# Kernel tuning notes

Hardware: AMD Instinct MI355X
Metric: run time of the kernel (lower is better)

## Reference

```python
import jax, jax.numpy as jnp
import numpy as np

B, T, N, C = 64, 8192, 16, 2
ONSET_PROB = 0.005  # sparse onsets, realistic for piano rolls


def setup_inputs() -> dict:
    key = jax.random.key(0)
    k1, k2 = jax.random.split(key)
    vals = jax.random.uniform(k1, (B, T, N, C), dtype=jnp.float32)
    mask = jax.random.uniform(k2, (B, T, N, 1)) < ONSET_PROB
    onsets = jnp.where(mask, vals, 0.0)  # mostly-zero onset roll
    return {"onsets": onsets}


def reference(onsets):
    # onsets: (b, t, n, c). onset flag per frame: any note's channel-0 > 0.
    b, t, n, c = onsets.shape
    onset = jnp.max(onsets[..., 0], axis=-1) > 0  # (b, t) bool
    # Recurrence state = (state + 1) * (1 - onset) counts frames since the
    # last onset (0 at an onset frame), with a virtual onset at index -1.
    # Closed form: out[i] = i - (index of most recent onset <= i, else -1).
    ar = jnp.arange(t, dtype=jnp.int32)  # (t,)
    idx = jnp.where(onset, ar[None, :], -1)  # (b, t)
    last = jax.lax.cummax(idx, axis=1)  # (b, t) last onset index so far
    out = (ar[None, :] - last).astype(onsets.dtype)[..., None]  # (b, t, 1)
    return out
```

## Files before the change

### kernel.cpp

```cpp
#include <hip/hip_runtime.h>

#define B_ 64
#define T_ 8192
#define N_ 16
#define C_ 2
#define TILE 256
#define NT (T_ / TILE)

__global__ __launch_bounds__(TILE) void k1_scan(const float* __restrict__ onsets,
                                                float* __restrict__ out,
                                                int* __restrict__ tileMax,
                                                int* __restrict__ firstOnset) {
    __shared__ int s[TILE];
    const int blk  = blockIdx.x;
    const int b    = blk / NT;
    const int tile = blk % NT;
    const int tid  = threadIdx.x;
    const int t    = tile * TILE + tid;

    const float4* p = (const float4*)onsets + (size_t)(b * T_ + t) * (N_ * C_ / 4);
    float m = 0.0f;
#pragma unroll
    for (int i = 0; i < 8; ++i) {
        float4 v = p[i];
        m = fmaxf(m, fmaxf(v.x, v.z));
    }
    const bool onset = (m > 0.0f);
    int idx = onset ? t : -1;

    s[tid] = idx;
    __syncthreads();
#pragma unroll
    for (int off = 1; off < TILE; off <<= 1) {
        int u = (tid >= off) ? s[tid - off] : -1;
        int v = s[tid];
        __syncthreads();
        s[tid] = (u > v) ? u : v;
        __syncthreads();
    }
    const int last = s[tid];
    out[b * T_ + t] = (float)(t - last);

    if (tid == TILE - 1) tileMax[blk] = last;

    s[tid] = onset ? t : 0x7fffffff;
    __syncthreads();
#pragma unroll
    for (int off = TILE / 2; off > 0; off >>= 1) {
        if (tid < off) {
            int a = s[tid], c = s[tid + off];
            s[tid] = (c < a) ? c : a;
        }
        __syncthreads();
    }
    if (tid == 0) firstOnset[blk] = s[0];
}

__global__ __launch_bounds__(TILE) void k2_fixup(const int* __restrict__ tileMax,
                                                 const int* __restrict__ firstOnset,
                                                 float* __restrict__ out) {
    const int blk  = blockIdx.x;
    const int b    = blk / NT;
    const int tile = blk % NT;
    const int tid  = threadIdx.x;

    __shared__ int red[NT];
    __shared__ int carry_s;
    if (tid < NT) red[tid] = -1;
    __syncthreads();
    if (tid < tile) red[tid] = tileMax[b * NT + tid];
    __syncthreads();
    if (tid == 0) {
        int c = -1;
#pragma unroll
        for (int i = 0; i < NT; ++i) c = (red[i] > c) ? red[i] : c;
        carry_s = c;
    }
    __syncthreads();

    const int f = firstOnset[blk];
    const int t = tile * TILE + tid;
    if (t < f) out[b * T_ + t] = (float)(t - carry_s);
}

extern "C" void kernel_launch(void* const* d_in, const int* in_sizes, int n_in,
                              void* d_out, int out_size, void* d_ws, size_t ws_size,
                              hipStream_t stream) {
    const float* onsets = (const float*)d_in[0];
    float* out = (float*)d_out;

    int* tileMax    = (int*)d_ws;
    int* firstOnset = tileMax + B_ * NT;

    dim3 grid(B_ * NT);
    k1_scan<<<grid, TILE, 0, stream>>>(onsets, out, tileMax, firstOnset);
    k2_fixup<<<grid, TILE, 0, stream>>>(tileMax, firstOnset, out);
}
```

Baseline: 99.57 us.

## Coalesce onset loads and replace shared-memory scans with wave shuffles

Each wave now reads contiguous float4 chunks: each group of 8 lanes covers one frame's 32 floats and reduces them with xor shuffles into a per-frame byte flag in shared memory. The 256-wide shared-memory Hillis-Steele scan and the tree min-reduction become a 64-lane shuffle scan, a ballot for the first onset, and a small per-wave carry combine. The fixup kernel also uses a shuffle reduction instead of a serial loop. Together these aim to improve load coalescing and cut the many __syncthreads barriers, at the cost of an extra shared-memory flag pass.

```diff
diff --git a/kernel.cpp b/kernel.cpp
--- a/kernel.cpp
+++ b/kernel.cpp
@@ -11,70 +11,83 @@
                                                 float* __restrict__ out,
                                                 int* __restrict__ tileMax,
                                                 int* __restrict__ firstOnset) {
-    __shared__ int s[TILE];
     const int blk  = blockIdx.x;
-    const int b    = blk / NT;
-    const int tile = blk % NT;
+    const int b    = blk >> 5;
+    const int tile = blk & (NT - 1);
     const int tid  = threadIdx.x;
-    const int t    = tile * TILE + tid;
+    const int wave = tid >> 6;
+    const int lane = tid & 63;
 
-    const float4* p = (const float4*)onsets + (size_t)(b * T_ + t) * (N_ * C_ / 4);
-    float m = 0.0f;
+    __shared__ unsigned char flags[TILE];
+    __shared__ int wmax[4];
+    __shared__ int wfirst[4];
+
+    const float4* base4 = (const float4*)onsets + ((size_t)(b * T_ + tile * TILE) << 3);
+
 #pragma unroll
-    for (int i = 0; i < 8; ++i) {
-        float4 v = p[i];
-        m = fmaxf(m, fmaxf(v.x, v.z));
+    for (int j = 0; j < 8; ++j) {
+        float4 v = base4[(wave << 9) + (j << 6) + lane];
+        float mm = fmaxf(v.x, v.z);
+        mm = fmaxf(mm, __shfl_xor(mm, 1));
+        mm = fmaxf(mm, __shfl_xor(mm, 2));
+        mm = fmaxf(mm, __shfl_xor(mm, 4));
+        if ((lane & 7) == 0)
+            flags[(wave << 6) + (j << 3) + (lane >> 3)] = (mm > 0.0f) ? 1 : 0;
     }
-    const bool onset = (m > 0.0f);
-    int idx = onset ? t : -1;
+    __syncthreads();
 
-    s[tid] = idx;
+    const int t  = tile * TILE + tid;
+    const bool on = flags[tid] != 0;
+    int idx = on ? t : -1;
+#pragma unroll
+    for (int off = 1; off < 64; off <<= 1) {
+        int u = __shfl_up(idx, off);
+        if (lane >= off) idx = (u > idx) ? u : idx;
+    }
+    if (lane == 63) wmax[wave] = idx;
+    unsigned long long bal = __ballot(on);
+    if (lane == 0)
+        wfirst[wave] = bal ? (tile * TILE + (wave << 6) + __ffsll(bal) - 1) : 0x7fffffff;
     __syncthreads();
+
+    int carry = -1;
 #pragma unroll
-    for (int off = 1; off < TILE; off <<= 1) {
-        int u = (tid >= off) ? s[tid - off] : -1;
-        int v = s[tid];
-        __syncthreads();
-        s[tid] = (u > v) ? u : v;
-        __syncthreads();
+    for (int w = 0; w < 4; ++w) {
+        int v = wmax[w];
+        if (w < wave && v > carry) carry = v;
     }
-    const int last = s[tid];
+    const int last = (carry > idx) ? carry : idx;
     out[b * T_ + t] = (float)(t - last);
 
-    if (tid == TILE - 1) tileMax[blk] = last;
-
-    s[tid] = onset ? t : 0x7fffffff;
-    __syncthreads();
+    if (tid == 0) {
+        int bm = wmax[0], f = wfirst[0];
 #pragma unroll
-    for (int off = TILE / 2; off > 0; off >>= 1) {
-        if (tid < off) {
-            int a = s[tid], c = s[tid + off];
-            s[tid] = (c < a) ? c : a;
+        for (int w = 1; w < 4; ++w) {
+            bm = (wmax[w] > bm) ? wmax[w] : bm;
+            f  = (wfirst[w] < f) ? wfirst[w] : f;
         }
-        __syncthreads();
+        tileMax[blk]    = bm;
+        firstOnset[blk] = f;
     }
-    if (tid == 0) firstOnset[blk] = s[0];
 }
 
 __global__ __launch_bounds__(TILE) void k2_fixup(const int* __restrict__ tileMax,
                                                  const int* __restrict__ firstOnset,
                                                  float* __restrict__ out) {
     const int blk  = blockIdx.x;
-    const int b    = blk / NT;
-    const int tile = blk % NT;
+    const int b    = blk >> 5;
+    const int tile = blk & (NT - 1);
     const int tid  = threadIdx.x;
 
-    __shared__ int red[NT];
     __shared__ int carry_s;
-    if (tid < NT) red[tid] = -1;
-    __syncthreads();
-    if (tid < tile) red[tid] = tileMax[b * NT + tid];
-    __syncthreads();
-    if (tid == 0) {
-        int c = -1;
+    if (tid < 64) {
+        int v = (tid < tile) ? tileMax[(b << 5) + tid] : -1;
 #pragma unroll
-        for (int i = 0; i < NT; ++i) c = (red[i] > c) ? red[i] : c;
-        carry_s = c;
+        for (int off = 32; off; off >>= 1) {
+            int u = __shfl_xor(v, off);
+            v = (u > v) ? u : v;
+        }
+        if (tid == 0) carry_s = v;
     }
     __syncthreads();
 
```

New measurement: 93.63 us. -6.0%, faster.
